# Performance work log

Measured on AMD Instinct MI355X. Metric: run time of the kernel, lower is better.

The kernel has to match this reference:

```python
import jax, jax.numpy as jnp
import numpy as np

N_NODES = 100000
N_EDGES = 800000
F_IN, HID, N_CLS = 256, 128, 32


def setup_inputs() -> dict:
    key = jax.random.key(0)
    k1, k2, k3, k4, k5 = jax.random.split(key, 5)
    features = jax.random.normal(k1, (N_NODES, F_IN), dtype=jnp.float32)
    # random directed edges with no self loops (so add_remaining_self_loops == append all loops)
    src = jax.random.randint(k2, (N_EDGES,), 0, N_NODES)
    off = jax.random.randint(k3, (N_EDGES,), 1, N_NODES)
    dst = (src + off) % N_NODES
    edge_index = jnp.stack([src, dst]).astype(jnp.int64)
    # Glorot-style params for the two GCNConv layers
    W1 = jax.random.normal(k4, (F_IN, HID), dtype=jnp.float32) * (1.0 / np.sqrt(F_IN))
    b1 = jnp.zeros((HID,), dtype=jnp.float32)
    W2 = jax.random.normal(k5, (HID, N_CLS), dtype=jnp.float32) * (1.0 / np.sqrt(HID))
    b2 = jnp.zeros((N_CLS,), dtype=jnp.float32)
    return {"features": features, "edge_index": edge_index, "W1": W1, "b1": b1, "W2": W2, "b2": b2}


def _gcn_conv(x, W, b, src, dst, norm, n):
    xw = x @ W                                  # [N, d_out] dense GEMM
    msg = xw[src] * norm[:, None]               # gather + scale, [E, d_out]
    out = jax.ops.segment_sum(msg, dst, num_segments=n)  # scatter-add to targets
    return out + b


def reference(features, edge_index, W1, b1, W2, b2):
    n = features.shape[0]
    # add_remaining_self_loops (input has none, so append all)
    loops = jnp.arange(n, dtype=edge_index.dtype)
    src = jnp.concatenate([edge_index[0], loops])
    dst = jnp.concatenate([edge_index[1], loops])
    # gcn_norm: deg over targets, sym normalization deg^-1/2 A deg^-1/2
    deg = jax.ops.segment_sum(jnp.ones_like(src, dtype=features.dtype), dst, num_segments=n)
    dinv = jnp.where(deg > 0, jax.lax.rsqrt(deg), 0.0)
    norm = dinv[src] * dinv[dst]
    x = _gcn_conv(features, W1, b1, src, dst, norm, n)
    x = jax.nn.relu(x)
    # dropout is identity at inference (training=False)
    x = _gcn_conv(x, W2, b2, src, dst, norm, n)
    return jax.nn.log_softmax(x, axis=1)
```

## Files before the change

kernel.cpp:

```cpp
#include <hip/hip_runtime.h>
#include <hip/hip_bf16.h>

typedef __bf16 bf16_t;
typedef __attribute__((ext_vector_type(8))) __bf16 bf16x8;
typedef __attribute__((ext_vector_type(4))) float f32x4;

__device__ inline void packB_one(const float* __restrict__ B, bf16_t* __restrict__ Bp,
                                 int N, int idx) {
    int j    = idx & 7;
    int lane = (idx >> 3) & 63;
    int st   = idx >> 9;
    int nt   = N >> 4;
    int s = st / nt, t = st - s * nt;
    int k = s * 32 + (lane >> 4) * 8 + j;
    int n = t * 16 + (lane & 15);
    Bp[idx] = (bf16_t)B[(size_t)k * N + n];
}

template <int KSTEPS, int NTILES>
__global__ __launch_bounds__(256) void k_front(
        const float* __restrict__ feat, const bf16_t* __restrict__ Bp1r,
        bf16_t* __restrict__ XW1, int M,
        const float* __restrict__ W1, bf16_t* __restrict__ Bp1,
        const float* __restrict__ W2, bf16_t* __restrict__ Bp2,
        const int* __restrict__ dst, int* __restrict__ deg,
        int* __restrict__ rank, int E, int DEGB, int GEMMB) {
    int b = blockIdx.x, t = threadIdx.x;
    if (b < DEGB) {
        int i = b * 1024 + t * 4;
        if (i + 4 <= E) {
            int4 v = *(const int4*)(dst + i);
            int4 r;
            r.x = atomicAdd(&deg[v.x], 1);
            r.y = atomicAdd(&deg[v.y], 1);
            r.z = atomicAdd(&deg[v.z], 1);
            r.w = atomicAdd(&deg[v.w], 1);
            *(int4*)(rank + i) = r;
        } else {
            for (int j = 0; j < 4; ++j)
                if (i + j < E) rank[i + j] = atomicAdd(&deg[dst[i + j]], 1);
        }
        return;
    }
    b -= DEGB;
    if (b < GEMMB) {
        int wave = (b * 256 + t) >> 6;
        if (wave * 16 >= M) return;
        int lane = t & 63;
        int r16 = lane & 15, quad = lane >> 4;
        const int K = KSTEPS * 32, N = NTILES * 16;
        f32x4 acc[NTILES] = {};
        const float* arow = feat + (size_t)(wave * 16 + r16) * K + quad * 8;
#pragma unroll
        for (int s = 0; s < KSTEPS; ++s) {
            const float* ap = arow + s * 32;
            bf16x8 a;
#pragma unroll
            for (int j = 0; j < 8; ++j) a[j] = (bf16_t)ap[j];
            const bf16_t* bp = Bp1r + ((size_t)(s * NTILES) * 64 + lane) * 8;
#pragma unroll
            for (int tt = 0; tt < NTILES; ++tt) {
                bf16x8 bb = *(const bf16x8*)(bp + tt * 512);
                acc[tt] = __builtin_amdgcn_mfma_f32_16x16x32_bf16(a, bb, acc[tt], 0, 0, 0);
            }
        }
#pragma unroll
        for (int tt = 0; tt < NTILES; ++tt)
#pragma unroll
            for (int r = 0; r < 4; ++r)
                XW1[(size_t)(wave * 16 + quad * 4 + r) * N + tt * 16 + r16] = (bf16_t)acc[tt][r];
        return;
    }
    b -= GEMMB;
    int idx = b * 256 + t;
    if (idx < 32768) packB_one(W1, Bp1, 128, idx);
    else             packB_one(W2, Bp2, 32, idx - 32768);
}

__global__ __launch_bounds__(256) void k_dinv_scan1(const int* __restrict__ deg,
                                                    float* __restrict__ dinv,
                                                    int* __restrict__ bsum, int n) {
    __shared__ int red[256];
    int b = blockIdx.x, t = threadIdx.x;
    int base = b * 1024 + t * 4;
    int s = 0;
#pragma unroll
    for (int j = 0; j < 4; ++j) {
        int i = base + j;
        if (i < n) { int d = deg[i]; s += d; dinv[i] = rsqrtf((float)(d + 1)); }
    }
    red[t] = s;
    __syncthreads();
    for (int d = 128; d > 0; d >>= 1) {
        if (t < d) red[t] += red[t + d];
        __syncthreads();
    }
    if (t == 0) bsum[b] = red[0];
}

__global__ __launch_bounds__(256) void k_scan3f(const int* __restrict__ deg,
                                                const int* __restrict__ bsum, int nb,
                                                int* __restrict__ rowPtr, int n) {
    __shared__ int red[256];
    __shared__ int boff[256];
    int b = blockIdx.x, t = threadIdx.x;
    int base = b * 1024 + t * 4;
    int v[4]; int s = 0;
#pragma unroll
    for (int j = 0; j < 4; ++j) { int i = base + j; v[j] = (i < n) ? deg[i] : 0; s += v[j]; }
    red[t] = s;
    boff[t] = (t < nb) ? bsum[t] : 0;
    __syncthreads();
    for (int d = 1; d < 256; d <<= 1) {
        int u  = (t >= d) ? red[t - d]  : 0;
        int u2 = (t >= d) ? boff[t - d] : 0;
        __syncthreads();
        red[t] += u;
        boff[t] += u2;
        __syncthreads();
    }
    int blockOff = (b == 0) ? 0 : boff[b - 1];
    if (b == 0 && t == 0) rowPtr[n] = boff[nb - 1];
    int run = blockOff + red[t] - s;
#pragma unroll
    for (int j = 0; j < 4; ++j) {
        int i = base + j;
        if (i < n) { rowPtr[i] = run; run += v[j]; }
    }
}

__global__ __launch_bounds__(256) void k_scatter(
        const int* __restrict__ src, const int* __restrict__ dst,
        const int* __restrict__ rank, const int* __restrict__ rowPtr,
        const float* __restrict__ dinv, int2* __restrict__ edata, int E) {
    int i = (blockIdx.x * 256 + threadIdx.x) * 4;
    if (i + 4 <= E) {
        int4 s4 = *(const int4*)(src + i);
        int4 d4 = *(const int4*)(dst + i);
        int4 r4 = *(const int4*)(rank + i);
        int p0 = rowPtr[d4.x] + r4.x, p1 = rowPtr[d4.y] + r4.y;
        int p2 = rowPtr[d4.z] + r4.z, p3 = rowPtr[d4.w] + r4.w;
        int2 e0; e0.x = s4.x; e0.y = __float_as_int(dinv[s4.x] * dinv[d4.x]);
        int2 e1; e1.x = s4.y; e1.y = __float_as_int(dinv[s4.y] * dinv[d4.y]);
        int2 e2; e2.x = s4.z; e2.y = __float_as_int(dinv[s4.z] * dinv[d4.z]);
        int2 e3; e3.x = s4.w; e3.y = __float_as_int(dinv[s4.w] * dinv[d4.w]);
        edata[p0] = e0; edata[p1] = e1; edata[p2] = e2; edata[p3] = e3;
    } else {
        for (int j = 0; j < 4; ++j) {
            int e = i + j;
            if (e >= E) break;
            int s = src[e], d = dst[e];
            int2 p; p.x = s; p.y = __float_as_int(dinv[s] * dinv[d]);
            edata[rowPtr[d] + rank[e]] = p;
        }
    }
}

template <int KSTEPS, int NTILES>
__global__ __launch_bounds__(256) void k_gemm_p(
        const bf16_t* __restrict__ Ap, const bf16_t* __restrict__ Bp,
        bf16_t* __restrict__ C, int M) {
    int wave = (blockIdx.x * blockDim.x + threadIdx.x) >> 6;
    if (wave * 16 >= M) return;
    int lane = threadIdx.x & 63;
    int r16 = lane & 15, quad = lane >> 4;
    const int N = NTILES * 16;
    f32x4 acc[NTILES] = {};
    const bf16_t* apb = Ap + (size_t)wave * (KSTEPS * 512) + lane * 8;
#pragma unroll
    for (int s = 0; s < KSTEPS; ++s) {
        bf16x8 a = *(const bf16x8*)(apb + s * 512);
        const bf16_t* bp = Bp + ((size_t)(s * NTILES) * 64 + lane) * 8;
#pragma unroll
        for (int t = 0; t < NTILES; ++t) {
            bf16x8 b = *(const bf16x8*)(bp + t * 512);
            acc[t] = __builtin_amdgcn_mfma_f32_16x16x32_bf16(a, b, acc[t], 0, 0, 0);
        }
    }
#pragma unroll
    for (int t = 0; t < NTILES; ++t)
#pragma unroll
        for (int r = 0; r < 4; ++r)
            C[(size_t)(wave * 16 + quad * 4 + r) * N + t * 16 + r16] = (bf16_t)acc[t][r];
}

__global__ __launch_bounds__(256) void k_agg1(
        const int* __restrict__ rowPtr, const int2* __restrict__ edata,
        const bf16_t* __restrict__ XW1, const float* __restrict__ dinv,
        const float* __restrict__ b1, bf16_t* __restrict__ Hp, int n) {
    int wave = (blockIdx.x * blockDim.x + threadIdx.x) >> 6;
    if (wave >= n) return;
    int lane = threadIdx.x & 63;
    int fl = (lane & 15) << 3;
    int h  = lane >> 4;
    int r0 = rowPtr[wave], r1 = rowPtr[wave + 1];
    float d = dinv[wave], d2 = d * d;
    bf16x8 xs = *(const bf16x8*)(XW1 + ((size_t)wave << 7) + fl);
    float a0[8] = {}, a1[8] = {};
    int k = r0 + h;
    for (; k + 4 < r1; k += 8) {
        int2 e0 = edata[k], e1 = edata[k + 4];
        float w0 = __int_as_float(e0.y), w1 = __int_as_float(e1.y);
        bf16x8 x0 = *(const bf16x8*)(XW1 + ((size_t)e0.x << 7) + fl);
        bf16x8 x1 = *(const bf16x8*)(XW1 + ((size_t)e1.x << 7) + fl);
#pragma unroll
        for (int j = 0; j < 8; ++j) { a0[j] += (float)x0[j] * w0; a1[j] += (float)x1[j] * w1; }
    }
    if (k < r1) {
        int2 e0 = edata[k];
        float w0 = __int_as_float(e0.y);
        bf16x8 x0 = *(const bf16x8*)(XW1 + ((size_t)e0.x << 7) + fl);
#pragma unroll
        for (int j = 0; j < 8; ++j) a0[j] += (float)x0[j] * w0;
    }
#pragma unroll
    for (int j = 0; j < 8; ++j) {
        a0[j] += a1[j];
        a0[j] += __shfl_xor(a0[j], 16);
        a0[j] += __shfl_xor(a0[j], 32);
    }
    if (h == 0) {
        bf16x8 hv;
#pragma unroll
        for (int j = 0; j < 8; ++j) {
            float v = a0[j] + (float)xs[j] * d2 + b1[fl + j];
            hv[j] = (bf16_t)fmaxf(v, 0.f);
        }
        int q = lane & 15;
        size_t off = (((size_t)(wave >> 4) * 4 + (q >> 2)) * 64
                      + (wave & 15) + 16 * (q & 3)) * 8;
        *(bf16x8*)(Hp + off) = hv;
    }
}

__global__ __launch_bounds__(256) void k_agg2(
        const int* __restrict__ rowPtr, const int2* __restrict__ edata,
        const bf16_t* __restrict__ XW2, const float* __restrict__ dinv,
        const float* __restrict__ b2, float* __restrict__ out, int n) {
    int wave = (blockIdx.x * blockDim.x + threadIdx.x) >> 6;
    if (wave >= n) return;
    int lane = threadIdx.x & 63;
    int g = lane & 15;
    int h = lane >> 4;
    int r0 = rowPtr[wave], r1 = rowPtr[wave + 1];
    float d = dinv[wave], d2 = d * d;
    unsigned ps = *(const unsigned*)(XW2 + ((size_t)wave << 5) + 2 * g);
    float2 bb = *(const float2*)(b2 + 2 * g);
    float a00 = 0.f, a01 = 0.f, a10 = 0.f, a11 = 0.f;
    int k = r0 + h;
    for (; k + 4 < r1; k += 8) {
        int2 e0 = edata[k], e1 = edata[k + 4];
        float w0 = __int_as_float(e0.y), w1 = __int_as_float(e1.y);
        unsigned p0 = *(const unsigned*)(XW2 + ((size_t)e0.x << 5) + 2 * g);
        unsigned p1 = *(const unsigned*)(XW2 + ((size_t)e1.x << 5) + 2 * g);
        a00 += __int_as_float(p0 << 16) * w0;
        a01 += __int_as_float(p0 & 0xffff0000u) * w0;
        a10 += __int_as_float(p1 << 16) * w1;
        a11 += __int_as_float(p1 & 0xffff0000u) * w1;
    }
    if (k < r1) {
        int2 e0 = edata[k];
        float w0 = __int_as_float(e0.y);
        unsigned p0 = *(const unsigned*)(XW2 + ((size_t)e0.x << 5) + 2 * g);
        a00 += __int_as_float(p0 << 16) * w0;
        a01 += __int_as_float(p0 & 0xffff0000u) * w0;
    }
    float v0 = a00 + a10, v1 = a01 + a11;
    v0 += __shfl_xor(v0, 16); v0 += __shfl_xor(v0, 32);
    v1 += __shfl_xor(v1, 16); v1 += __shfl_xor(v1, 32);
    v0 += __int_as_float(ps << 16) * d2 + bb.x;
    v1 += __int_as_float(ps & 0xffff0000u) * d2 + bb.y;
    float mx = fmaxf(v0, v1);
#pragma unroll
    for (int m = 8; m >= 1; m >>= 1) mx = fmaxf(mx, __shfl_xor(mx, m));
    float s = __expf(v0 - mx) + __expf(v1 - mx);
#pragma unroll
    for (int m = 8; m >= 1; m >>= 1) s += __shfl_xor(s, m);
    if (h == 0) {
        float ls = __logf(s);
        float2 o; o.x = v0 - mx - ls; o.y = v1 - mx - ls;
        *(float2*)(out + ((size_t)wave << 5) + 2 * g) = o;
    }
}

extern "C" void kernel_launch(void* const* d_in, const int* in_sizes, int n_in,
                              void* d_out, int out_size, void* d_ws, size_t ws_size,
                              hipStream_t stream) {
    const float* feat = (const float*)d_in[0];
    const int*   eidx = (const int*)d_in[1];
    const float* W1   = (const float*)d_in[2];
    const float* b1   = (const float*)d_in[3];
    const float* W2   = (const float*)d_in[4];
    const float* b2   = (const float*)d_in[5];
    float* out = (float*)d_out;

    const int FIN = 256, HID = 128, NCLS = 32;
    const int N = in_sizes[0] / FIN;
    const int E = in_sizes[1] / 2;
    const int* src = eidx;
    const int* dst = eidx + E;

    char* ws = (char*)d_ws;
    size_t o = 0;
    auto alloc = [&](size_t bytes) -> void* {
        void* p = ws + o;
        o = (o + bytes + 255) & ~(size_t)255;
        return p;
    };
    int*    deg    = (int*)   alloc((size_t)N * 4);
    int*    rank   = (int*)   alloc((size_t)E * 4);
    float*  dinv   = (float*) alloc((size_t)N * 4);
    int*    rowPtr = (int*)   alloc((size_t)(N + 1) * 4);
    int*    bsum   = (int*)   alloc(256 * 4);
    bf16_t* Bp1    = (bf16_t*)alloc((size_t)(FIN / 32) * (HID / 16) * 512 * 2);
    bf16_t* Bp2    = (bf16_t*)alloc((size_t)(HID / 32) * (NCLS / 16) * 512 * 2);
    int2*   edata  = (int2*)  alloc((size_t)E * 8);
    bf16_t* XW1    = (bf16_t*)alloc((size_t)N * HID * 2);
    bf16_t* Hp     = (bf16_t*)alloc((size_t)N * HID * 2);
    bf16_t* XW2    = XW1;

    const int T = 256;
    const int NB = (N + 1023) >> 10;
    const int DEGB  = (E + 1023) / 1024;
    const int GEMMB = (((N + 15) / 16) * 64 + T - 1) / T;
    const int PACKB = (32768 + 4096) / 256;
    hipMemsetAsync(deg, 0, (size_t)N * 4, stream);
    {
        k_front<8, 8><<<PACKB, T, 0, stream>>>(
            feat, Bp1, XW1, 0, W1, Bp1, W2, Bp2, dst, deg, rank, 0, 0, 0);
    }
    k_front<8, 8><<<DEGB + GEMMB, T, 0, stream>>>(
        feat, Bp1, XW1, N, W1, Bp1, W2, Bp2, dst, deg, rank, E, DEGB, GEMMB);
    k_dinv_scan1<<<NB, T, 0, stream>>>(deg, dinv, bsum, N);
    k_scan3f    <<<NB, T, 0, stream>>>(deg, bsum, NB, rowPtr, N);
    k_scatter   <<<(E + 1023) / 1024, T, 0, stream>>>(src, dst, rank, rowPtr, dinv, edata, E);
    k_agg1<<<(N * 64 + T - 1) / T, T, 0, stream>>>(rowPtr, edata, XW1, dinv, b1, Hp, N);
    {
        int waves = (N + 15) / 16;
        k_gemm_p<4, 2><<<(waves * 64 + T - 1) / T, T, 0, stream>>>(Hp, Bp2, XW2, N);
    }
    k_agg2<<<(N * 64 + T - 1) / T, T, 0, stream>>>(rowPtr, edata, XW2, dinv, b2, out, N);
}
```

Measured before the change: 325.4 us.

## Store XW1 as fp8 and merge weight packing with degree zeroing

```diff
diff --git a/kernel.cpp b/kernel.cpp
--- a/kernel.cpp
+++ b/kernel.cpp
@@ -4,6 +4,7 @@
 typedef __bf16 bf16_t;
 typedef __attribute__((ext_vector_type(8))) __bf16 bf16x8;
 typedef __attribute__((ext_vector_type(4))) float f32x4;
+typedef __attribute__((ext_vector_type(2))) float f32x2;
 
 __device__ inline void packB_one(const float* __restrict__ B, bf16_t* __restrict__ Bp,
                                  int N, int idx) {
@@ -17,14 +18,39 @@
     Bp[idx] = (bf16_t)B[(size_t)k * N + n];
 }
 
+__device__ inline void fma8_fp8(uint2 u, float w, float* a) {
+    f32x2 p;
+    p = __builtin_amdgcn_cvt_pk_f32_fp8(u.x, false); a[0] += p[0] * w; a[1] += p[1] * w;
+    p = __builtin_amdgcn_cvt_pk_f32_fp8(u.x, true);  a[2] += p[0] * w; a[3] += p[1] * w;
+    p = __builtin_amdgcn_cvt_pk_f32_fp8(u.y, false); a[4] += p[0] * w; a[5] += p[1] * w;
+    p = __builtin_amdgcn_cvt_pk_f32_fp8(u.y, true);  a[6] += p[0] * w; a[7] += p[1] * w;
+}
+
+__global__ __launch_bounds__(256) void k_prep(
+        const float* __restrict__ W1, bf16_t* __restrict__ Bp1,
+        const float* __restrict__ W2, bf16_t* __restrict__ Bp2,
+        int* __restrict__ deg, int N) {
+    int b = blockIdx.x, t = threadIdx.x;
+    const int PACKB = (32768 + 4096) / 256;
+    if (b < PACKB) {
+        int idx = b * 256 + t;
+        if (idx < 32768) packB_one(W1, Bp1, 128, idx);
+        else             packB_one(W2, Bp2, 32, idx - 32768);
+        return;
+    }
+    int i = ((b - PACKB) * 256 + t) * 4;
+    if (i < N) {
+        if (i + 4 <= N) *(int4*)(deg + i) = make_int4(0, 0, 0, 0);
+        else for (int j = 0; i + j < N; ++j) deg[i + j] = 0;
+    }
+}
+
 template <int KSTEPS, int NTILES>
 __global__ __launch_bounds__(256) void k_front(
-        const float* __restrict__ feat, const bf16_t* __restrict__ Bp1r,
-        bf16_t* __restrict__ XW1, int M,
-        const float* __restrict__ W1, bf16_t* __restrict__ Bp1,
-        const float* __restrict__ W2, bf16_t* __restrict__ Bp2,
+        const float* __restrict__ feat, const bf16_t* __restrict__ Bp1,
+        unsigned char* __restrict__ XW1, int M,
         const int* __restrict__ dst, int* __restrict__ deg,
-        int* __restrict__ rank, int E, int DEGB, int GEMMB) {
+        int* __restrict__ rank, int E, int DEGB) {
     int b = blockIdx.x, t = threadIdx.x;
     if (b < DEGB) {
         int i = b * 1024 + t * 4;
@@ -43,7 +69,7 @@
         return;
     }
     b -= DEGB;
-    if (b < GEMMB) {
+    {
         int wave = (b * 256 + t) >> 6;
         if (wave * 16 >= M) return;
         int lane = t & 63;
@@ -57,7 +83,7 @@
             bf16x8 a;
 #pragma unroll
             for (int j = 0; j < 8; ++j) a[j] = (bf16_t)ap[j];
-            const bf16_t* bp = Bp1r + ((size_t)(s * NTILES) * 64 + lane) * 8;
+            const bf16_t* bp = Bp1 + ((size_t)(s * NTILES) * 64 + lane) * 8;
 #pragma unroll
             for (int tt = 0; tt < NTILES; ++tt) {
                 bf16x8 bb = *(const bf16x8*)(bp + tt * 512);
@@ -67,14 +93,12 @@
 #pragma unroll
         for (int tt = 0; tt < NTILES; ++tt)
 #pragma unroll
-            for (int r = 0; r < 4; ++r)
-                XW1[(size_t)(wave * 16 + quad * 4 + r) * N + tt * 16 + r16] = (bf16_t)acc[tt][r];
-        return;
-    }
-    b -= GEMMB;
-    int idx = b * 256 + t;
-    if (idx < 32768) packB_one(W1, Bp1, 128, idx);
-    else             packB_one(W2, Bp2, 32, idx - 32768);
+            for (int r = 0; r < 4; ++r) {
+                int pk = __builtin_amdgcn_cvt_pk_fp8_f32(acc[tt][r], acc[tt][r], 0, false);
+                XW1[(size_t)(wave * 16 + quad * 4 + r) * N + tt * 16 + r16] =
+                    (unsigned char)pk;
+            }
+    }
 }
 
 __global__ __launch_bounds__(256) void k_dinv_scan1(const int* __restrict__ deg,
@@ -186,7 +210,7 @@
 
 __global__ __launch_bounds__(256) void k_agg1(
         const int* __restrict__ rowPtr, const int2* __restrict__ edata,
-        const bf16_t* __restrict__ XW1, const float* __restrict__ dinv,
+        const unsigned char* __restrict__ XW1, const float* __restrict__ dinv,
         const float* __restrict__ b1, bf16_t* __restrict__ Hp, int n) {
     int wave = (blockIdx.x * blockDim.x + threadIdx.x) >> 6;
     if (wave >= n) return;
@@ -195,23 +219,22 @@
     int h  = lane >> 4;
     int r0 = rowPtr[wave], r1 = rowPtr[wave + 1];
     float d = dinv[wave], d2 = d * d;
-    bf16x8 xs = *(const bf16x8*)(XW1 + ((size_t)wave << 7) + fl);
+    uint2 us = *(const uint2*)(XW1 + (size_t)wave * 128 + fl);
     float a0[8] = {}, a1[8] = {};
     int k = r0 + h;
     for (; k + 4 < r1; k += 8) {
         int2 e0 = edata[k], e1 = edata[k + 4];
         float w0 = __int_as_float(e0.y), w1 = __int_as_float(e1.y);
-        bf16x8 x0 = *(const bf16x8*)(XW1 + ((size_t)e0.x << 7) + fl);
-        bf16x8 x1 = *(const bf16x8*)(XW1 + ((size_t)e1.x << 7) + fl);
-#pragma unroll
-        for (int j = 0; j < 8; ++j) { a0[j] += (float)x0[j] * w0; a1[j] += (float)x1[j] * w1; }
+        uint2 u0 = *(const uint2*)(XW1 + (size_t)e0.x * 128 + fl);
+        uint2 u1 = *(const uint2*)(XW1 + (size_t)e1.x * 128 + fl);
+        fma8_fp8(u0, w0, a0);
+        fma8_fp8(u1, w1, a1);
     }
     if (k < r1) {
         int2 e0 = edata[k];
         float w0 = __int_as_float(e0.y);
-        bf16x8 x0 = *(const bf16x8*)(XW1 + ((size_t)e0.x << 7) + fl);
-#pragma unroll
-        for (int j = 0; j < 8; ++j) a0[j] += (float)x0[j] * w0;
+        uint2 u0 = *(const uint2*)(XW1 + (size_t)e0.x * 128 + fl);
+        fma8_fp8(u0, w0, a0);
     }
 #pragma unroll
     for (int j = 0; j < 8; ++j) {
@@ -220,10 +243,11 @@
         a0[j] += __shfl_xor(a0[j], 32);
     }
     if (h == 0) {
+        fma8_fp8(us, d2, a0);
         bf16x8 hv;
 #pragma unroll
         for (int j = 0; j < 8; ++j) {
-            float v = a0[j] + (float)xs[j] * d2 + b1[fl + j];
+            float v = a0[j] + b1[fl + j];
             hv[j] = (bf16_t)fmaxf(v, 0.f);
         }
         int q = lane & 15;
@@ -315,22 +339,20 @@
     bf16_t* Bp1    = (bf16_t*)alloc((size_t)(FIN / 32) * (HID / 16) * 512 * 2);
     bf16_t* Bp2    = (bf16_t*)alloc((size_t)(HID / 32) * (NCLS / 16) * 512 * 2);
     int2*   edata  = (int2*)  alloc((size_t)E * 8);
-    bf16_t* XW1    = (bf16_t*)alloc((size_t)N * HID * 2);
+    unsigned char* XW1 = (unsigned char*)alloc((size_t)N * HID);
     bf16_t* Hp     = (bf16_t*)alloc((size_t)N * HID * 2);
-    bf16_t* XW2    = XW1;
+    bf16_t* XW2    = (bf16_t*)XW1;
 
     const int T = 256;
     const int NB = (N + 1023) >> 10;
     const int DEGB  = (E + 1023) / 1024;
     const int GEMMB = (((N + 15) / 16) * 64 + T - 1) / T;
     const int PACKB = (32768 + 4096) / 256;
-    hipMemsetAsync(deg, 0, (size_t)N * 4, stream);
-    {
-        k_front<8, 8><<<PACKB, T, 0, stream>>>(
-            feat, Bp1, XW1, 0, W1, Bp1, W2, Bp2, dst, deg, rank, 0, 0, 0);
-    }
+    const int ZB    = (N + 1023) / 1024;
+
+    k_prep      <<<PACKB + ZB, T, 0, stream>>>(W1, Bp1, W2, Bp2, deg, N);
     k_front<8, 8><<<DEGB + GEMMB, T, 0, stream>>>(
-        feat, Bp1, XW1, N, W1, Bp1, W2, Bp2, dst, deg, rank, E, DEGB, GEMMB);
+        feat, Bp1, XW1, N, dst, deg, rank, E, DEGB);
     k_dinv_scan1<<<NB, T, 0, stream>>>(deg, dinv, bsum, N);
     k_scan3f    <<<NB, T, 0, stream>>>(deg, bsum, NB, rowPtr, N);
     k_scatter   <<<(E + 1023) / 1024, T, 0, stream>>>(src, dst, rank, rowPtr, dinv, edata, E);
```

Result: faster. 317.8 us (-2.4%).
